# Performance work log

Hardware: AMD Instinct MI355X
Metric: run time of the kernel (lower is better)

The kernel has to match this reference:

```python
import jax, jax.numpy as jnp
import numpy as np
import math

D_MODEL = 1024
NUM_HEADS = 16
D_K = D_MODEL // NUM_HEADS
B, S = 4, 2048


def setup_inputs() -> dict:
    key = jax.random.key(0)
    ks = jax.random.split(key, 12)
    q = jax.random.normal(ks[0], (B, S, D_MODEL), dtype=jnp.float32)
    k = jax.random.normal(ks[1], (B, S, D_MODEL), dtype=jnp.float32)
    v = jax.random.normal(ks[2], (B, S, D_MODEL), dtype=jnp.float32)
    # causal mask: True where attention is disallowed (masked_fill semantics)
    mask = jnp.triu(jnp.ones((S, S), dtype=bool), k=1)
    # xavier_uniform_ for projection weights, torch Linear default for biases
    limit = math.sqrt(6.0 / (D_MODEL + D_MODEL))
    def xavier(kk):
        return jax.random.uniform(kk, (D_MODEL, D_MODEL), jnp.float32, -limit, limit)
    blim = 1.0 / math.sqrt(D_MODEL)
    def bias(kk):
        return jax.random.uniform(kk, (D_MODEL,), jnp.float32, -blim, blim)
    return {
        "q": q, "k": k, "v": v, "mask": mask,
        "wq": xavier(ks[3]), "bq": bias(ks[4]),
        "wk": xavier(ks[5]), "bk": bias(ks[6]),
        "wv": xavier(ks[7]), "bv": bias(ks[8]),
        "wo": xavier(ks[9]), "bo": bias(ks[10]),
    }


def reference(q, k, v, mask, wq, bq, wk, bk, wv, bv, wo, bo):
    b = q.shape[0]
    # torch Linear: y = x @ W.T + b
    def proj(x, w, bb):
        return (jnp.einsum('bsd,ed->bse', x, w) + bb).reshape(b, -1, NUM_HEADS, D_K).transpose(0, 2, 1, 3)
    qh = proj(q, wq, bq)  # [B,H,S,d_k]
    kh = proj(k, wk, bk)
    vh = proj(v, wv, bv)
    scores = jnp.einsum('bhqd,bhkd->bhqk', qh, kh) / math.sqrt(D_K)
    scores = jnp.where(mask, jnp.float32(-1e9), scores)
    probs = jax.nn.softmax(scores, axis=-1)  # dropout p=0 -> identity
    out = jnp.einsum('bhqk,bhkd->bhqd', probs, vh)
    out = out.transpose(0, 2, 1, 3).reshape(b, -1, D_MODEL)
    return jnp.einsum('bsd,ed->bse', out, wo) + bo
```

## Files before the change

### kernel.cpp

```cpp
#include <hip/hip_runtime.h>
#include <hip/hip_bf16.h>
#include <math.h>

#define S_LEN 2048
#define DM    1024
#define NH    16
#define DKH   64
#define NEG_BIG (-1e30f)
#define QSCALE 0.18033688f

typedef __bf16 bf16_t;
typedef bf16_t bf16x8 __attribute__((ext_vector_type(8)));
typedef bf16_t bf16x4 __attribute__((ext_vector_type(4)));
typedef bf16_t bf16x2 __attribute__((ext_vector_type(2)));
typedef float  f32x4  __attribute__((ext_vector_type(4)));

__device__ __forceinline__ void gload16(const void* g, void* l) {
    __builtin_amdgcn_global_load_lds((const __attribute__((address_space(1))) void*)g,
                                     (__attribute__((address_space(3))) void*)l, 16, 0, 0);
}

__device__ __forceinline__ unsigned pack2(float a, float b) {
    bf16x2 v; v[0] = (bf16_t)a; v[1] = (bf16_t)b;
    return __builtin_bit_cast(unsigned, v);
}

__device__ __forceinline__ bf16x8 cvt8v(f32x4 a, f32x4 b) {
    bf16x8 v;
    v[0] = (bf16_t)a[0]; v[1] = (bf16_t)a[1]; v[2] = (bf16_t)a[2]; v[3] = (bf16_t)a[3];
    v[4] = (bf16_t)b[0]; v[5] = (bf16_t)b[1]; v[6] = (bf16_t)b[2]; v[7] = (bf16_t)b[3];
    return v;
}

__global__ __launch_bounds__(256) void cvt4_w(const float* __restrict__ w0, const float* __restrict__ w1,
                                              const float* __restrict__ w2, const float* __restrict__ w3,
                                              bf16_t* __restrict__ o0, bf16_t* __restrict__ o1,
                                              bf16_t* __restrict__ o2, bf16_t* __restrict__ o3) {
    const float* in; bf16_t* out;
    switch (blockIdx.y) {
        case 0: in = w0; out = o0; break;
        case 1: in = w1; out = o1; break;
        case 2: in = w2; out = o2; break;
        default: in = w3; out = o3; break;
    }
    int i = (blockIdx.x * 256 + threadIdx.x) * 4;
    float4 f = *(const float4*)(in + i);
    bf16x4 v;
    v[0] = (bf16_t)f.x; v[1] = (bf16_t)f.y; v[2] = (bf16_t)f.z; v[3] = (bf16_t)f.w;
    *(bf16x4*)(out + i) = v;
}

template<int EPI>
__global__ __launch_bounds__(256) void gemm_proj(const float* __restrict__ Af,
                                                 const bf16_t* __restrict__ B,
                                                 const float* __restrict__ bias,
                                                 bf16_t* __restrict__ Out,
                                                 float oscale) {
    __shared__ float  AsF[3][128 * 32];
    __shared__ bf16_t Bs[3][128 * 32];

    const int d    = blockIdx.x;
    const int orig = (d & 7) * 64 + (d >> 3);
    const int mBase = (orig >> 3) * 128;
    const int nBase = (orig & 7) * 128;

    const int tid  = threadIdx.x;
    const int w    = tid >> 6;
    const int lane = tid & 63;
    const int g    = lane >> 4;
    const int r    = lane & 15;
    const int wm   = w >> 1, wn = w & 1;

    const int srow = lane >> 2;
    const int scol = (lane & 3) * 8;
    const int frow = lane >> 3;
    const int fsl  = (lane & 7) ^ (frow & 7);

    auto stage = [&](int buf, int kt) {
        #pragma unroll
        for (int c = 0; c < 4; ++c) {
            const int row = w * 32 + c * 8;
            gload16(Af + (size_t)(mBase + row + frow) * 1024 + kt + fsl * 4, &AsF[buf][row * 32]);
        }
        #pragma unroll
        for (int c = 0; c < 2; ++c) {
            const int row = w * 32 + c * 16;
            gload16(B + (size_t)(nBase + row + srow) * 1024 + kt + scol, &Bs[buf][row * 32]);
        }
    };

    auto compute = [&](int buf, f32x4 (*acc)[4]) {
        bf16x8 af[4], bfr[4];
        #pragma unroll
        for (int i = 0; i < 4; i++) {
            const int R = wm * 64 + i * 16 + r;
            const float* rb = &AsF[buf][R * 32];
            f32x4 f0 = *(const f32x4*)(rb + (((2 * g) ^ (r & 7)) << 2));
            f32x4 f1 = *(const f32x4*)(rb + (((2 * g + 1) ^ (r & 7)) << 2));
            af[i] = cvt8v(f0, f1);
        }
        #pragma unroll
        for (int i = 0; i < 4; i++)
            bfr[i] = *(const bf16x8*)&Bs[buf][(wn * 64 + i * 16 + r) * 32 + g * 8];
        #pragma unroll
        for (int mi = 0; mi < 4; mi++)
            #pragma unroll
            for (int ni = 0; ni < 4; ni++)
                acc[mi][ni] = __builtin_amdgcn_mfma_f32_16x16x32_bf16(
                    af[mi], bfr[ni], acc[mi][ni], 0, 0, 0);
    };

    f32x4 acc[4][4] = {};

    stage(0, 0);
    stage(1, 32);

    int cur = 0;
    for (int t = 0; t < 31; ++t) {
        asm volatile("s_waitcnt vmcnt(6)" ::: "memory");
        __builtin_amdgcn_s_barrier();
        compute(cur, acc);
        if (t + 2 < 32) stage((cur + 2) % 3, (t + 2) * 32);
        cur = (cur + 1) % 3;
    }
    asm volatile("s_waitcnt vmcnt(0)" ::: "memory");
    __builtin_amdgcn_s_barrier();
    compute(cur, acc);

    #pragma unroll
    for (int ni = 0; ni < 4; ni++) {
        const int n = nBase + wn * 64 + ni * 16 + r;
        const float bn = bias[n];
        #pragma unroll
        for (int mi = 0; mi < 4; mi++) {
            #pragma unroll
            for (int qq = 0; qq < 4; qq++) {
                int m = mBase + wm * 64 + mi * 16 + g * 4 + qq;
                float val = (acc[mi][ni][qq] + bn) * oscale;
                int b = m >> 11, s = m & 2047;
                int hh = n >> 6, dd = n & 63;
                bf16_t bvv = (bf16_t)val;
                if constexpr (EPI == 0) {
                    Out[(((size_t)(b * NH + hh)) * S_LEN + s) * DKH + dd] = bvv;
                } else {
                    int o = s & 63;
                    int c2 = (o & 0x23) | (((o >> 3) & 1) << 4) | (((o >> 2) & 1) << 3)
                           | (((o >> 4) & 1) << 2);
                    int s2 = (s & ~63) | c2;
                    Out[(((size_t)(b * NH + hh)) * DKH + dd) * S_LEN + s2] = bvv;
                }
            }
        }
    }
}

__global__ __launch_bounds__(256) void gemm_o(const bf16_t* __restrict__ A,
                                              const bf16_t* __restrict__ B,
                                              const float* __restrict__ bias,
                                              float* __restrict__ Out) {
    __shared__ bf16_t As[3][128 * 32];
    __shared__ bf16_t Bs[3][128 * 32];

    const int d    = blockIdx.x;
    const int orig = (d & 7) * 64 + (d >> 3);
    const int mBase = (orig >> 3) * 128;
    const int nBase = (orig & 7) * 128;

    const int tid  = threadIdx.x;
    const int w    = tid >> 6;
    const int lane = tid & 63;
    const int g    = lane >> 4;
    const int r    = lane & 15;
    const int wm   = w >> 1, wn = w & 1;

    const int srow = lane >> 2;
    const int scol = (lane & 3) * 8;

    auto stage = [&](int buf, int kt) {
        #pragma unroll
        for (int c = 0; c < 2; ++c) {
            const int row = w * 32 + c * 16;
            gload16(A + (size_t)(mBase + row + srow) * 1024 + kt + scol, &As[buf][row * 32]);
            gload16(B + (size_t)(nBase + row + srow) * 1024 + kt + scol, &Bs[buf][row * 32]);
        }
    };

    auto compute = [&](int buf, f32x4 (*acc)[4]) {
        bf16x8 af[4], bfr[4];
        #pragma unroll
        for (int i = 0; i < 4; i++)
            af[i] = *(const bf16x8*)&As[buf][(wm * 64 + i * 16 + r) * 32 + g * 8];
        #pragma unroll
        for (int i = 0; i < 4; i++)
            bfr[i] = *(const bf16x8*)&Bs[buf][(wn * 64 + i * 16 + r) * 32 + g * 8];
        #pragma unroll
        for (int mi = 0; mi < 4; mi++)
            #pragma unroll
            for (int ni = 0; ni < 4; ni++)
                acc[mi][ni] = __builtin_amdgcn_mfma_f32_16x16x32_bf16(
                    af[mi], bfr[ni], acc[mi][ni], 0, 0, 0);
    };

    f32x4 acc[4][4] = {};

    stage(0, 0);
    stage(1, 32);

    int cur = 0;
    for (int t = 0; t < 31; ++t) {
        asm volatile("s_waitcnt vmcnt(4)" ::: "memory");
        __builtin_amdgcn_s_barrier();
        compute(cur, acc);
        if (t + 2 < 32) stage((cur + 2) % 3, (t + 2) * 32);
        cur = (cur + 1) % 3;
    }
    asm volatile("s_waitcnt vmcnt(0)" ::: "memory");
    __builtin_amdgcn_s_barrier();
    compute(cur, acc);

    #pragma unroll
    for (int ni = 0; ni < 4; ni++) {
        const int n = nBase + wn * 64 + ni * 16 + r;
        const float bn = bias[n];
        #pragma unroll
        for (int mi = 0; mi < 4; mi++) {
            #pragma unroll
            for (int qq = 0; qq < 4; qq++) {
                int m = mBase + wm * 64 + mi * 16 + g * 4 + qq;
                Out[(size_t)m * 1024 + n] = acc[mi][ni][qq] + bn;
            }
        }
    }
}

__device__ __forceinline__ void tile_softmax(f32x4 s[4], bool diag, int kbase, int qg,
                                             int g, bf16x8 pf[2]) {
    unsigned P32[8];
    #pragma unroll
    for (int ni = 0; ni < 4; ++ni) {
        float p[4];
        #pragma unroll
        for (int e = 0; e < 4; ++e) {
            float xx = s[ni][e];
            if (diag) {
                int kk = kbase + ni * 16 + g * 4 + e;
                if (kk > qg) xx = NEG_BIG;
            }
            p[e] = __builtin_amdgcn_exp2f(xx);
        }
        P32[2 * ni]     = pack2(p[0], p[1]);
        P32[2 * ni + 1] = pack2(p[2], p[3]);
    }
    union U { unsigned u[4]; bf16x8 v; } u0, u1;
    u0.u[0] = P32[0]; u0.u[1] = P32[1]; u0.u[2] = P32[2]; u0.u[3] = P32[3];
    u1.u[0] = P32[4]; u1.u[1] = P32[5]; u1.u[2] = P32[6]; u1.u[3] = P32[7];
    pf[0] = u0.v;
    pf[1] = u1.v;
}

__global__ __launch_bounds__(256) void attn9_kernel(const bf16_t* __restrict__ Qh,
                                                    const bf16_t* __restrict__ Kh,
                                                    const bf16_t* __restrict__ Vt,
                                                    bf16_t* __restrict__ Out) {
    __shared__ bf16_t KV[2][2][64][64];

    const int j   = blockIdx.x;
    const int c   = j >> 8;
    const int rem = j & 255;
    const int y   = rem >> 6;
    const int bh  = rem & 63;
    const int p   = (c == 0) ? y : (c == 1) ? 15 - y : (c == 2) ? 4 + y : 11 - y;

    const int b   = bh >> 4, h = bh & 15;
    const int tid = threadIdx.x;
    const int w    = tid >> 6;
    const int lane = tid & 63;
    const int g    = lane >> 4;
    const int r    = lane & 15;

    const int qtA = 2 * p, qtB = 2 * p + 1, last = qtB;

    const bf16_t* Qg = Qh + (size_t)bh * S_LEN * DKH;
    const bf16_t* Kg = Kh + (size_t)bh * S_LEN * DKH;
    const bf16_t* Vg = Vt + (size_t)bh * DKH * S_LEN;

    const int qA = qtA * 64 + w * 16 + r;
    const int qB = qtB * 64 + w * 16 + r;

    bf16x8 qfA[2], qfB[2];
    #pragma unroll
    for (int hh = 0; hh < 2; ++hh) {
        qfA[hh] = *(const bf16x8*)(Qg + (size_t)qA * DKH + hh * 32 + g * 8);
        qfB[hh] = *(const bf16x8*)(Qg + (size_t)qB * DKH + hh * 32 + g * 8);
    }

    bf16x8 ones;
    #pragma unroll
    for (int jj = 0; jj < 8; ++jj) ones[jj] = (bf16_t)1.0f;

    auto stage = [&](int buf, int kt) {
        #pragma unroll
        for (int cc = 0; cc < 2; ++cc) {
            const int row = w * 16 + cc * 8 + (lane >> 3);
            const int sl  = (lane & 7) ^ (row & 7);
            gload16(Kg + ((size_t)(kt * 64 + row)) * DKH + sl * 8,
                    (char*)&KV[buf][0][0][0] + w * 2048 + cc * 1024);
            gload16(Vg + (size_t)row * S_LEN + kt * 64 + sl * 8,
                    (char*)&KV[buf][1][0][0] + w * 2048 + cc * 1024);
        }
    };

    f32x4 oA[4] = {}, oB[4] = {};
    f32x4 lA4 = {}, lB4 = {};

    stage(0, 0);
    asm volatile("s_waitcnt vmcnt(0)" ::: "memory");
    __builtin_amdgcn_s_barrier();

    for (int kt = 0; kt <= last; ++kt) {
        const int buf = kt & 1;
        if (kt < last) stage(buf ^ 1, kt + 1);

        bf16x8 kf[4][2];
        #pragma unroll
        for (int ni = 0; ni < 4; ++ni) {
            const int row = ni * 16 + r;
            const char* base = (const char*)&KV[buf][0][0][0] + (row << 7);
            kf[ni][0] = *(const bf16x8*)(base + (((0 + g) ^ (row & 7)) << 4));
            kf[ni][1] = *(const bf16x8*)(base + (((4 + g) ^ (row & 7)) << 4));
        }

        const bool actA = (kt <= qtA);
        bf16x8 pfA[2], pfB[2];

        if (actA) {
            f32x4 s[4] = {};
            __builtin_amdgcn_s_setprio(1);
            #pragma unroll
            for (int ni = 0; ni < 4; ++ni) {
                s[ni] = __builtin_amdgcn_mfma_f32_16x16x32_bf16(kf[ni][0], qfA[0], s[ni], 0, 0, 0);
                s[ni] = __builtin_amdgcn_mfma_f32_16x16x32_bf16(kf[ni][1], qfA[1], s[ni], 0, 0, 0);
            }
            __builtin_amdgcn_s_setprio(0);
            tile_softmax(s, kt == qtA, kt * 64, qA, g, pfA);
        }
        {
            f32x4 s[4] = {};
            __builtin_amdgcn_s_setprio(1);
            #pragma unroll
            for (int ni = 0; ni < 4; ++ni) {
                s[ni] = __builtin_amdgcn_mfma_f32_16x16x32_bf16(kf[ni][0], qfB[0], s[ni], 0, 0, 0);
                s[ni] = __builtin_amdgcn_mfma_f32_16x16x32_bf16(kf[ni][1], qfB[1], s[ni], 0, 0, 0);
            }
            __builtin_amdgcn_s_setprio(0);
            tile_softmax(s, kt == qtB, kt * 64, qB, g, pfB);
        }

        __builtin_amdgcn_s_setprio(1);
        #pragma unroll
        for (int ndi = 0; ndi < 4; ++ndi) {
            const int row = ndi * 16 + r;
            const char* base = (const char*)&KV[buf][1][0][0] + (row << 7);
            bf16x8 v0 = *(const bf16x8*)(base + (((0 + g) ^ (row & 7)) << 4));
            bf16x8 v1 = *(const bf16x8*)(base + (((4 + g) ^ (row & 7)) << 4));
            if (actA) {
                oA[ndi] = __builtin_amdgcn_mfma_f32_16x16x32_bf16(v0, pfA[0], oA[ndi], 0, 0, 0);
                oA[ndi] = __builtin_amdgcn_mfma_f32_16x16x32_bf16(v1, pfA[1], oA[ndi], 0, 0, 0);
            }
            oB[ndi] = __builtin_amdgcn_mfma_f32_16x16x32_bf16(v0, pfB[0], oB[ndi], 0, 0, 0);
            oB[ndi] = __builtin_amdgcn_mfma_f32_16x16x32_bf16(v1, pfB[1], oB[ndi], 0, 0, 0);
        }
        if (actA) {
            lA4 = __builtin_amdgcn_mfma_f32_16x16x32_bf16(ones, pfA[0], lA4, 0, 0, 0);
            lA4 = __builtin_amdgcn_mfma_f32_16x16x32_bf16(ones, pfA[1], lA4, 0, 0, 0);
        }
        lB4 = __builtin_amdgcn_mfma_f32_16x16x32_bf16(ones, pfB[0], lB4, 0, 0, 0);
        lB4 = __builtin_amdgcn_mfma_f32_16x16x32_bf16(ones, pfB[1], lB4, 0, 0, 0);
        __builtin_amdgcn_s_setprio(0);

        asm volatile("s_waitcnt vmcnt(0)" ::: "memory");
        __builtin_amdgcn_s_barrier();
    }

    const float invA = 1.0f / lA4[0], invB = 1.0f / lB4[0];
    bf16_t* OutA = Out + ((size_t)(b * S_LEN + qA)) * DM + h * DKH;
    bf16_t* OutB = Out + ((size_t)(b * S_LEN + qB)) * DM + h * DKH;
    #pragma unroll
    for (int ndi = 0; ndi < 4; ++ndi) {
        bf16x4 pa, pb;
        #pragma unroll
        for (int e = 0; e < 4; ++e) {
            pa[e] = (bf16_t)(oA[ndi][e] * invA);
            pb[e] = (bf16_t)(oB[ndi][e] * invB);
        }
        *(bf16x4*)(OutA + ndi * 16 + g * 4) = pa;
        *(bf16x4*)(OutB + ndi * 16 + g * 4) = pb;
    }
}

extern "C" void kernel_launch(void* const* d_in, const int* in_sizes, int n_in,
                              void* d_out, int out_size, void* d_ws, size_t ws_size,
                              hipStream_t stream) {
    const float* q  = (const float*)d_in[0];
    const float* k  = (const float*)d_in[1];
    const float* v  = (const float*)d_in[2];
    const float* wq = (const float*)d_in[4];
    const float* bq = (const float*)d_in[5];
    const float* wk = (const float*)d_in[6];
    const float* bk = (const float*)d_in[7];
    const float* wv = (const float*)d_in[8];
    const float* bv = (const float*)d_in[9];
    const float* wo = (const float*)d_in[10];
    const float* bo = (const float*)d_in[11];
    float* out = (float*)d_out;

    bf16_t* ws   = (bf16_t*)d_ws;
    bf16_t* Wq   = ws;
    bf16_t* Wk   = Wq + (1 << 20);
    bf16_t* Wv   = Wk + (1 << 20);
    bf16_t* Wo   = Wv + (1 << 20);
    bf16_t* Qh   = Wo + (1 << 20);
    bf16_t* Kh   = Qh + (8 << 20);
    bf16_t* Vt   = Kh + (8 << 20);
    bf16_t* attn = Vt + (8 << 20);

    cvt4_w<<<dim3(1024, 4), 256, 0, stream>>>(wq, wk, wv, wo, Wq, Wk, Wv, Wo);

    gemm_proj<0><<<512, 256, 0, stream>>>(q, Wq, bq, Qh, QSCALE);
    gemm_proj<0><<<512, 256, 0, stream>>>(k, Wk, bk, Kh, 1.0f);
    gemm_proj<1><<<512, 256, 0, stream>>>(v, Wv, bv, Vt, 1.0f);

    attn9_kernel<<<1024, 256, 0, stream>>>(Qh, Kh, Vt, attn);

    gemm_o<<<512, 256, 0, stream>>>(attn, Wo, bo, out);
}
```

Before: 165.0 us.

## Process four query tiles per block to reuse staged K/V tiles

Each attention block now handles four consecutive 64-row query tiles instead of two, so every K/V tile staged into LDS is reused by up to four query tiles. The grid halves to 512 blocks, with chunks paired (x and 7-x) to balance causal work. This cuts global K/V traffic and per-tile barrier overhead. In exchange it raises register pressure (four sets of accumulators and Q fragments), may lower occupancy, and gives fewer blocks for load balancing across CUs.

```diff
diff --git a/kernel.cpp b/kernel.cpp
--- a/kernel.cpp
+++ b/kernel.cpp
@@ -258,18 +258,16 @@
     pf[1] = u1.v;
 }
 
-__global__ __launch_bounds__(256) void attn9_kernel(const bf16_t* __restrict__ Qh,
-                                                    const bf16_t* __restrict__ Kh,
-                                                    const bf16_t* __restrict__ Vt,
-                                                    bf16_t* __restrict__ Out) {
+__global__ __launch_bounds__(256) void attn10_kernel(const bf16_t* __restrict__ Qh,
+                                                     const bf16_t* __restrict__ Kh,
+                                                     const bf16_t* __restrict__ Vt,
+                                                     bf16_t* __restrict__ Out) {
     __shared__ bf16_t KV[2][2][64][64];
 
-    const int j   = blockIdx.x;
-    const int c   = j >> 8;
-    const int rem = j & 255;
-    const int y   = rem >> 6;
-    const int bh  = rem & 63;
-    const int p   = (c == 0) ? y : (c == 1) ? 15 - y : (c == 2) ? 4 + y : 11 - y;
+    const int j     = blockIdx.x;
+    const int bh    = j & 63;
+    const int chunk = j >> 6;
+    const int x     = (chunk < 4) ? chunk : 11 - chunk;
 
     const int b   = bh >> 4, h = bh & 15;
     const int tid = threadIdx.x;
@@ -278,20 +276,21 @@
     const int g    = lane >> 4;
     const int r    = lane & 15;
 
-    const int qtA = 2 * p, qtB = 2 * p + 1, last = qtB;
+    const int qt0  = 4 * x;
+    const int last = 4 * x + 3;
 
     const bf16_t* Qg = Qh + (size_t)bh * S_LEN * DKH;
     const bf16_t* Kg = Kh + (size_t)bh * S_LEN * DKH;
     const bf16_t* Vg = Vt + (size_t)bh * DKH * S_LEN;
 
-    const int qA = qtA * 64 + w * 16 + r;
-    const int qB = qtB * 64 + w * 16 + r;
-
-    bf16x8 qfA[2], qfB[2];
-    #pragma unroll
-    for (int hh = 0; hh < 2; ++hh) {
-        qfA[hh] = *(const bf16x8*)(Qg + (size_t)qA * DKH + hh * 32 + g * 8);
-        qfB[hh] = *(const bf16x8*)(Qg + (size_t)qB * DKH + hh * 32 + g * 8);
+    int q_[4];
+    bf16x8 qf[4][2];
+    #pragma unroll
+    for (int t = 0; t < 4; ++t) {
+        q_[t] = (qt0 + t) * 64 + w * 16 + r;
+        #pragma unroll
+        for (int hh = 0; hh < 2; ++hh)
+            qf[t][hh] = *(const bf16x8*)(Qg + (size_t)q_[t] * DKH + hh * 32 + g * 8);
     }
 
     bf16x8 ones;
@@ -310,8 +309,8 @@
         }
     };
 
-    f32x4 oA[4] = {}, oB[4] = {};
-    f32x4 lA4 = {}, lB4 = {};
+    f32x4 o[4][4] = {};
+    f32x4 l4[4] = {};
 
     stage(0, 0);
     asm volatile("s_waitcnt vmcnt(0)" ::: "memory");
@@ -321,80 +320,60 @@
         const int buf = kt & 1;
         if (kt < last) stage(buf ^ 1, kt + 1);
 
-        bf16x8 kf[4][2];
+        bf16x8 kf[4][2], vf[4][2];
         #pragma unroll
         for (int ni = 0; ni < 4; ++ni) {
             const int row = ni * 16 + r;
-            const char* base = (const char*)&KV[buf][0][0][0] + (row << 7);
-            kf[ni][0] = *(const bf16x8*)(base + (((0 + g) ^ (row & 7)) << 4));
-            kf[ni][1] = *(const bf16x8*)(base + (((4 + g) ^ (row & 7)) << 4));
-        }
-
-        const bool actA = (kt <= qtA);
-        bf16x8 pfA[2], pfB[2];
-
-        if (actA) {
-            f32x4 s[4] = {};
-            __builtin_amdgcn_s_setprio(1);
-            #pragma unroll
-            for (int ni = 0; ni < 4; ++ni) {
-                s[ni] = __builtin_amdgcn_mfma_f32_16x16x32_bf16(kf[ni][0], qfA[0], s[ni], 0, 0, 0);
-                s[ni] = __builtin_amdgcn_mfma_f32_16x16x32_bf16(kf[ni][1], qfA[1], s[ni], 0, 0, 0);
+            const char* kb = (const char*)&KV[buf][0][0][0] + (row << 7);
+            const char* vb = (const char*)&KV[buf][1][0][0] + (row << 7);
+            kf[ni][0] = *(const bf16x8*)(kb + (((0 + g) ^ (row & 7)) << 4));
+            kf[ni][1] = *(const bf16x8*)(kb + (((4 + g) ^ (row & 7)) << 4));
+            vf[ni][0] = *(const bf16x8*)(vb + (((0 + g) ^ (row & 7)) << 4));
+            vf[ni][1] = *(const bf16x8*)(vb + (((4 + g) ^ (row & 7)) << 4));
+        }
+
+        #pragma unroll
+        for (int t = 0; t < 4; ++t) {
+            const int qt = qt0 + t;
+            if (kt <= qt) {
+                f32x4 s[4] = {};
+                __builtin_amdgcn_s_setprio(1);
+                #pragma unroll
+                for (int ni = 0; ni < 4; ++ni) {
+                    s[ni] = __builtin_amdgcn_mfma_f32_16x16x32_bf16(kf[ni][0], qf[t][0], s[ni], 0, 0, 0);
+                    s[ni] = __builtin_amdgcn_mfma_f32_16x16x32_bf16(kf[ni][1], qf[t][1], s[ni], 0, 0, 0);
+                }
+                __builtin_amdgcn_s_setprio(0);
+                bf16x8 pf[2];
+                tile_softmax(s, kt == qt, kt * 64, q_[t], g, pf);
+                __builtin_amdgcn_s_setprio(1);
+                #pragma unroll
+                for (int ndi = 0; ndi < 4; ++ndi) {
+                    o[t][ndi] = __builtin_amdgcn_mfma_f32_16x16x32_bf16(vf[ndi][0], pf[0], o[t][ndi], 0, 0, 0);
+                    o[t][ndi] = __builtin_amdgcn_mfma_f32_16x16x32_bf16(vf[ndi][1], pf[1], o[t][ndi], 0, 0, 0);
+                }
+                l4[t] = __builtin_amdgcn_mfma_f32_16x16x32_bf16(ones, pf[0], l4[t], 0, 0, 0);
+                l4[t] = __builtin_amdgcn_mfma_f32_16x16x32_bf16(ones, pf[1], l4[t], 0, 0, 0);
+                __builtin_amdgcn_s_setprio(0);
             }
-            __builtin_amdgcn_s_setprio(0);
-            tile_softmax(s, kt == qtA, kt * 64, qA, g, pfA);
-        }
-        {
-            f32x4 s[4] = {};
-            __builtin_amdgcn_s_setprio(1);
-            #pragma unroll
-            for (int ni = 0; ni < 4; ++ni) {
-                s[ni] = __builtin_amdgcn_mfma_f32_16x16x32_bf16(kf[ni][0], qfB[0], s[ni], 0, 0, 0);
-                s[ni] = __builtin_amdgcn_mfma_f32_16x16x32_bf16(kf[ni][1], qfB[1], s[ni], 0, 0, 0);
-            }
-            __builtin_amdgcn_s_setprio(0);
-            tile_softmax(s, kt == qtB, kt * 64, qB, g, pfB);
-        }
-
-        __builtin_amdgcn_s_setprio(1);
-        #pragma unroll
-        for (int ndi = 0; ndi < 4; ++ndi) {
-            const int row = ndi * 16 + r;
-            const char* base = (const char*)&KV[buf][1][0][0] + (row << 7);
-            bf16x8 v0 = *(const bf16x8*)(base + (((0 + g) ^ (row & 7)) << 4));
-            bf16x8 v1 = *(const bf16x8*)(base + (((4 + g) ^ (row & 7)) << 4));
-            if (actA) {
-                oA[ndi] = __builtin_amdgcn_mfma_f32_16x16x32_bf16(v0, pfA[0], oA[ndi], 0, 0, 0);
-                oA[ndi] = __builtin_amdgcn_mfma_f32_16x16x32_bf16(v1, pfA[1], oA[ndi], 0, 0, 0);
-            }
-            oB[ndi] = __builtin_amdgcn_mfma_f32_16x16x32_bf16(v0, pfB[0], oB[ndi], 0, 0, 0);
-            oB[ndi] = __builtin_amdgcn_mfma_f32_16x16x32_bf16(v1, pfB[1], oB[ndi], 0, 0, 0);
-        }
-        if (actA) {
-            lA4 = __builtin_amdgcn_mfma_f32_16x16x32_bf16(ones, pfA[0], lA4, 0, 0, 0);
-            lA4 = __builtin_amdgcn_mfma_f32_16x16x32_bf16(ones, pfA[1], lA4, 0, 0, 0);
-        }
-        lB4 = __builtin_amdgcn_mfma_f32_16x16x32_bf16(ones, pfB[0], lB4, 0, 0, 0);
-        lB4 = __builtin_amdgcn_mfma_f32_16x16x32_bf16(ones, pfB[1], lB4, 0, 0, 0);
-        __builtin_amdgcn_s_setprio(0);
+        }
 
         asm volatile("s_waitcnt vmcnt(0)" ::: "memory");
         __builtin_amdgcn_s_barrier();
     }
 
-    const float invA = 1.0f / lA4[0], invB = 1.0f / lB4[0];
-    bf16_t* OutA = Out + ((size_t)(b * S_LEN + qA)) * DM + h * DKH;
-    bf16_t* OutB = Out + ((size_t)(b * S_LEN + qB)) * DM + h * DKH;
-    #pragma unroll
-    for (int ndi = 0; ndi < 4; ++ndi) {
-        bf16x4 pa, pb;
-        #pragma unroll
-        for (int e = 0; e < 4; ++e) {
-            pa[e] = (bf16_t)(oA[ndi][e] * invA);
-            pb[e] = (bf16_t)(oB[ndi][e] * invB);
-        }
-        *(bf16x4*)(OutA + ndi * 16 + g * 4) = pa;
-        *(bf16x4*)(OutB + ndi * 16 + g * 4) = pb;
+    #pragma unroll
+    for (int t = 0; t < 4; ++t) {
+        const float inv = 1.0f / l4[t][0];
+        bf16_t* Op = Out + ((size_t)(b * S_LEN + q_[t])) * DM + h * DKH;
+        #pragma unroll
+        for (int ndi = 0; ndi < 4; ++ndi) {
+            bf16x4 pa;
+            #pragma unroll
+            for (int e = 0; e < 4; ++e)
+                pa[e] = (bf16_t)(o[t][ndi][e] * inv);
+            *(bf16x4*)(Op + ndi * 16 + g * 4) = pa;
+        }
     }
 }
 
@@ -430,7 +409,7 @@
     gemm_proj<0><<<512, 256, 0, stream>>>(k, Wk, bk, Kh, 1.0f);
     gemm_proj<1><<<512, 256, 0, stream>>>(v, Wv, bv, Vt, 1.0f);
 
-    attn9_kernel<<<1024, 256, 0, stream>>>(Qh, Kh, Vt, attn);
+    attn10_kernel<<<512, 256, 0, stream>>>(Qh, Kh, Vt, attn);
 
     gemm_o<<<512, 256, 0, stream>>>(attn, Wo, bo, out);
 }
```

After: 195.1 us. 18.2% more time.

## Split long causal attention rows into two KV chunks with atomic-flag merge

Applied to the files above, without the earlier changes.

The heaviest query-tile pairs (p>=8) are split across two blocks, each covering half of the KV range. Each block writes fp32 partial outputs and row sums to workspace, and the last block to arrive, found through an atomic counter, merges both halves and writes the output. The launch grows from 1024 to 1536 blocks and is meant to balance the causal workload and shorten the tail. The cost is extra global traffic for partials, an extra memset, and a softmax merge that assumes no running max (fixed exponent base).

```diff
diff --git a/kernel.cpp b/kernel.cpp
--- a/kernel.cpp
+++ b/kernel.cpp
@@ -258,18 +258,26 @@
     pf[1] = u1.v;
 }
 
-__global__ __launch_bounds__(256) void attn9_kernel(const bf16_t* __restrict__ Qh,
-                                                    const bf16_t* __restrict__ Kh,
-                                                    const bf16_t* __restrict__ Vt,
-                                                    bf16_t* __restrict__ Out) {
+#define PART_STRIDE 8448
+
+__global__ __launch_bounds__(256) void attn11_kernel(const bf16_t* __restrict__ Qh,
+                                                     const bf16_t* __restrict__ Kh,
+                                                     const bf16_t* __restrict__ Vt,
+                                                     bf16_t* __restrict__ Out,
+                                                     float* __restrict__ Opart,
+                                                     unsigned* __restrict__ flags) {
     __shared__ bf16_t KV[2][2][64][64];
-
-    const int j   = blockIdx.x;
-    const int c   = j >> 8;
-    const int rem = j & 255;
-    const int y   = rem >> 6;
-    const int bh  = rem & 63;
-    const int p   = (c == 0) ? y : (c == 1) ? 15 - y : (c == 2) ? 4 + y : 11 - y;
+    __shared__ int s_old;
+
+    const int slot = blockIdx.x >> 6;
+    const int bh   = blockIdx.x & 63;
+    int p, chunk, lo, hi; bool split;
+    if (slot < 16) {
+        p = 15 - (slot >> 1); chunk = slot & 1; split = true;
+        if (chunk == 0) { lo = 0; hi = p; } else { lo = p + 1; hi = 2 * p + 1; }
+    } else {
+        p = 23 - slot; chunk = 0; split = false; lo = 0; hi = 2 * p + 1;
+    }
 
     const int b   = bh >> 4, h = bh & 15;
     const int tid = threadIdx.x;
@@ -278,7 +286,7 @@
     const int g    = lane >> 4;
     const int r    = lane & 15;
 
-    const int qtA = 2 * p, qtB = 2 * p + 1, last = qtB;
+    const int qtA = 2 * p, qtB = 2 * p + 1;
 
     const bf16_t* Qg = Qh + (size_t)bh * S_LEN * DKH;
     const bf16_t* Kg = Kh + (size_t)bh * S_LEN * DKH;
@@ -313,13 +321,13 @@
     f32x4 oA[4] = {}, oB[4] = {};
     f32x4 lA4 = {}, lB4 = {};
 
-    stage(0, 0);
+    stage(lo & 1, lo);
     asm volatile("s_waitcnt vmcnt(0)" ::: "memory");
     __builtin_amdgcn_s_barrier();
 
-    for (int kt = 0; kt <= last; ++kt) {
+    for (int kt = lo; kt <= hi; ++kt) {
         const int buf = kt & 1;
-        if (kt < last) stage(buf ^ 1, kt + 1);
+        if (kt < hi) stage(buf ^ 1, kt + 1);
 
         bf16x8 kf[4][2];
         #pragma unroll
@@ -382,19 +390,68 @@
         __builtin_amdgcn_s_barrier();
     }
 
-    const float invA = 1.0f / lA4[0], invB = 1.0f / lB4[0];
+    const int qrow = w * 16 + r;
+
+    if (!split) {
+        const float invA = 1.0f / lA4[0], invB = 1.0f / lB4[0];
+        bf16_t* OutA = Out + ((size_t)(b * S_LEN + qA)) * DM + h * DKH;
+        bf16_t* OutB = Out + ((size_t)(b * S_LEN + qB)) * DM + h * DKH;
+        #pragma unroll
+        for (int ndi = 0; ndi < 4; ++ndi) {
+            bf16x4 pa, pb;
+            #pragma unroll
+            for (int e = 0; e < 4; ++e) {
+                pa[e] = (bf16_t)(oA[ndi][e] * invA);
+                pb[e] = (bf16_t)(oB[ndi][e] * invB);
+            }
+            *(bf16x4*)(OutA + ndi * 16 + g * 4) = pa;
+            *(bf16x4*)(OutB + ndi * 16 + g * 4) = pb;
+        }
+        return;
+    }
+
+    const int pairid = bh * 8 + (p - 8);
+    float* base = Opart + (size_t)(pairid * 2 + chunk) * PART_STRIDE;
+    #pragma unroll
+    for (int ndi = 0; ndi < 4; ++ndi) {
+        float* pA = base + 0    + qrow * 64 + ndi * 16 + g * 4;
+        float* pB = base + 4096 + qrow * 64 + ndi * 16 + g * 4;
+        #pragma unroll
+        for (int e = 0; e < 4; ++e) {
+            __hip_atomic_store(pA + e, oA[ndi][e], __ATOMIC_RELAXED, __HIP_MEMORY_SCOPE_AGENT);
+            __hip_atomic_store(pB + e, oB[ndi][e], __ATOMIC_RELAXED, __HIP_MEMORY_SCOPE_AGENT);
+        }
+    }
+    if (g == 0) {
+        __hip_atomic_store(base + 8192 + qrow,      lA4[0], __ATOMIC_RELAXED, __HIP_MEMORY_SCOPE_AGENT);
+        __hip_atomic_store(base + 8192 + 64 + qrow, lB4[0], __ATOMIC_RELAXED, __HIP_MEMORY_SCOPE_AGENT);
+    }
+    __syncthreads();
+    if (tid == 0)
+        s_old = (int)__hip_atomic_fetch_add(&flags[pairid], 1u, __ATOMIC_ACQ_REL, __HIP_MEMORY_SCOPE_AGENT);
+    __syncthreads();
+    if (s_old == 0) return;
+
+    const float* pb2 = Opart + (size_t)(pairid * 2 + (chunk ^ 1)) * PART_STRIDE;
+    float lA = lA4[0] + __hip_atomic_load(pb2 + 8192 + qrow, __ATOMIC_RELAXED, __HIP_MEMORY_SCOPE_AGENT);
+    float lB = lB4[0] + __hip_atomic_load(pb2 + 8192 + 64 + qrow, __ATOMIC_RELAXED, __HIP_MEMORY_SCOPE_AGENT);
+    const float invA = 1.0f / lA, invB = 1.0f / lB;
     bf16_t* OutA = Out + ((size_t)(b * S_LEN + qA)) * DM + h * DKH;
     bf16_t* OutB = Out + ((size_t)(b * S_LEN + qB)) * DM + h * DKH;
     #pragma unroll
     for (int ndi = 0; ndi < 4; ++ndi) {
-        bf16x4 pa, pb;
+        const float* rA = pb2 + 0    + qrow * 64 + ndi * 16 + g * 4;
+        const float* rB = pb2 + 4096 + qrow * 64 + ndi * 16 + g * 4;
+        bf16x4 pa, pbv;
         #pragma unroll
         for (int e = 0; e < 4; ++e) {
-            pa[e] = (bf16_t)(oA[ndi][e] * invA);
-            pb[e] = (bf16_t)(oB[ndi][e] * invB);
+            float a2 = oA[ndi][e] + __hip_atomic_load(rA + e, __ATOMIC_RELAXED, __HIP_MEMORY_SCOPE_AGENT);
+            float b2 = oB[ndi][e] + __hip_atomic_load(rB + e, __ATOMIC_RELAXED, __HIP_MEMORY_SCOPE_AGENT);
+            pa[e]  = (bf16_t)(a2 * invA);
+            pbv[e] = (bf16_t)(b2 * invB);
         }
         *(bf16x4*)(OutA + ndi * 16 + g * 4) = pa;
-        *(bf16x4*)(OutB + ndi * 16 + g * 4) = pb;
+        *(bf16x4*)(OutB + ndi * 16 + g * 4) = pbv;
     }
 }
 
@@ -423,6 +480,10 @@
     bf16_t* Kh   = Qh + (8 << 20);
     bf16_t* Vt   = Kh + (8 << 20);
     bf16_t* attn = Vt + (8 << 20);
+    float*  Opart = (float*)(attn + (8 << 20));
+    unsigned* flags = (unsigned*)(Opart + (size_t)512 * 2 * PART_STRIDE);
+
+    hipMemsetAsync(flags, 0, 512 * sizeof(unsigned), stream);
 
     cvt4_w<<<dim3(1024, 4), 256, 0, stream>>>(wq, wk, wv, wo, Wq, Wk, Wv, Wo);
 
@@ -430,7 +491,7 @@
     gemm_proj<0><<<512, 256, 0, stream>>>(k, Wk, bk, Kh, 1.0f);
     gemm_proj<1><<<512, 256, 0, stream>>>(v, Wv, bv, Vt, 1.0f);
 
-    attn9_kernel<<<1024, 256, 0, stream>>>(Qh, Kh, Vt, attn);
+    attn11_kernel<<<1536, 256, 0, stream>>>(Qh, Kh, Vt, attn, Opart, flags);
 
     gemm_o<<<512, 256, 0, stream>>>(attn, Wo, bo, out);
 }
```

Measured after the change: 272.7 us. 65.2% more time.
